# Kernel tuning notes

Measured on AMD Instinct MI355X. Metric: run time of the kernel, lower is better.

The kernel has to match this reference:

```python
import jax, jax.numpy as jnp
import numpy as np

B, S, D, A = 32, 2048, 512, 256


def setup_inputs() -> dict:
    key = jax.random.key(0)
    ks = jax.random.split(key, 9)
    enc = jax.random.normal(ks[0], (B, S, D), dtype=jnp.float32)
    dec = jax.random.normal(ks[1], (B, 1, D), dtype=jnp.float32)
    prev = jax.random.uniform(ks[2], (B, S), dtype=jnp.float32)
    prev = prev / jnp.sum(prev, axis=1, keepdims=True)  # normalized prev attention
    noise = jax.random.normal(ks[3], (B, S), dtype=jnp.float32)
    W = jax.random.normal(ks[4], (A, D), dtype=jnp.float32) / np.sqrt(D)
    V = jax.random.normal(ks[5], (A, D), dtype=jnp.float32) / np.sqrt(D)
    b = jax.random.normal(ks[6], (A,), dtype=jnp.float32)
    v_w = jax.random.normal(ks[7], (1, A), dtype=jnp.float32)
    v_g = jnp.full((1,), np.sqrt(1.0 / A), dtype=jnp.float32)  # weight_norm g init
    v_bias = jax.random.normal(ks[8], (1,), dtype=jnp.float32)
    r = jnp.full((1,), -4.0, dtype=jnp.float32)
    return {"encoder_outputs": enc, "decoder_h": dec, "prev_alpha": prev,
            "noise": noise, "W": W, "V": V, "b": b, "v_w": v_w,
            "v_g": v_g, "v_bias": v_bias, "r": r}


def reference(encoder_outputs, decoder_h, prev_alpha, noise, W, V, b, v_w, v_g, v_bias, r):
    # Energy: tanh-MLP Bahdanau score with weight-normed output projection
    h = jnp.tanh(jnp.einsum('bsd,ad->bsa', encoder_outputs, W)
                 + jnp.einsum('bod,ad->boa', decoder_h, V)  # [B,1,A] broadcasts over S
                 + b)
    w_eff = v_g * v_w / jnp.linalg.norm(v_w)       # weight_norm: g * v / ||v||
    energy = jnp.einsum('bsa,oa->bso', h, w_eff)[..., 0] + v_bias[0] + r[0]  # [B,S]
    # Soft monotonic attention recurrence
    p_select = jax.nn.sigmoid(energy + noise)
    log1mp = jnp.log(jnp.clip(1.0 - p_select, 1e-10, 1.0))
    cumprod_1mp = jnp.exp(jnp.cumsum(log1mp, axis=1))  # safe_cumprod
    alpha = p_select * cumprod_1mp * jnp.cumsum(prev_alpha / cumprod_1mp, axis=1)
    # Context: enc^T @ alpha
    context = jnp.einsum('bsd,bs->bd', encoder_outputs, alpha)
    return context, alpha
```

## Files before the change

kernel.cpp:

```cpp
#include <hip/hip_runtime.h>
#include <math.h>

#define B_  32
#define S_  2048
#define D_  512
#define A_  256
#define BS_ (B_ * S_)

#define WEFF_OFF  0
#define DEC_OFF   256
#define EPART_OFF 8448
#define CTX_OFF   (8448 + BS_)

typedef _Float16 f16x8 __attribute__((ext_vector_type(8)));
typedef __fp16   fp16x2 __attribute__((ext_vector_type(2)));
typedef _Float16 half4 __attribute__((ext_vector_type(4)));
typedef float floatx4 __attribute__((ext_vector_type(4)));

__device__ __forceinline__ void glds16(const void* g, void* l) {
    __builtin_amdgcn_global_load_lds(
        (const __attribute__((address_space(1))) void*)g,
        (__attribute__((address_space(3))) void*)l, 16, 0, 0);
}

__global__ void ma_prep_kernel(const float* __restrict__ v_w,
                               const float* __restrict__ v_g,
                               const float* __restrict__ dec,
                               const float* __restrict__ V,
                               const float* __restrict__ bvec,
                               const float* __restrict__ W,
                               _Float16* __restrict__ W16,
                               float* __restrict__ ws) {
    __shared__ float sh[D_];
    const int bid = blockIdx.x, t = threadIdx.x;
    if (bid == 0) {
        float v = v_w[t];
        float sq = v * v;
        #pragma unroll
        for (int off = 32; off > 0; off >>= 1) sq += __shfl_down(sq, off, 64);
        if ((t & 63) == 0) sh[t >> 6] = sq;
        __syncthreads();
        float n2 = sh[0] + sh[1] + sh[2] + sh[3];
        ws[WEFF_OFF + t] = v_g[0] * v / sqrtf(n2);
    } else if (bid <= B_) {
        const int b = bid - 1;
        sh[t]       = dec[b * D_ + t];
        sh[t + 256] = dec[b * D_ + 256 + t];
        __syncthreads();
        const float4* Vr = (const float4*)(V + (size_t)t * D_);
        float acc = 0.f;
        #pragma unroll 4
        for (int k = 0; k < D_ / 4; ++k) {
            float4 v4 = Vr[k];
            acc = fmaf(v4.x, sh[4*k+0], acc);
            acc = fmaf(v4.y, sh[4*k+1], acc);
            acc = fmaf(v4.z, sh[4*k+2], acc);
            acc = fmaf(v4.w, sh[4*k+3], acc);
        }
        ws[DEC_OFF + b * A_ + t] = acc + bvec[t];
    } else {
        int i = (bid - (B_ + 1)) * 256 + t;
        float4 v = ((const float4*)W)[i];
        half4 h;
        h[0] = (_Float16)v.x; h[1] = (_Float16)v.y;
        h[2] = (_Float16)v.z; h[3] = (_Float16)v.w;
        ((half4*)W16)[i] = h;
    }
}

__global__ __launch_bounds__(512) void ma_energy_mfma(
        const float* __restrict__ enc,
        const _Float16* __restrict__ W16,
        const float* __restrict__ ws_in,
        float* __restrict__ energy) {
    __shared__ __align__(16) char smem[81920];
    float*    const Asm = (float*)smem;
    _Float16* const Bsm = (_Float16*)(smem + 49152);

    const int t  = threadIdx.x;
    const int bx = blockIdx.x;
    const size_t R0 = (size_t)bx * 128;
    const int batch = bx >> 4;

    const int lane = t & 63, wid = t >> 6;
    const int wm = wid >> 2, wn = wid & 3;
    const int fr = lane & 15, kq = lane >> 4;

    const int arow = t >> 3, ac = t & 7;
    const float* AgS0 = enc + (R0 + (size_t)arow) * D_ + (ac ^ (arow & 7)) * 4;
    const float* AgS1 = AgS0 + (size_t)64 * D_;
    const int brow = t >> 2, bc = t & 3;
    const _Float16* BgS0 = W16 + (size_t)brow * D_ + (bc ^ ((brow >> 1) & 3)) * 8;
    const _Float16* BgS1 = BgS0 + (size_t)128 * D_;

    const int axc0 = ((2 * kq)     ^ (fr & 7)) * 4;
    const int axc1 = ((2 * kq + 1) ^ (fr & 7)) * 4;
    const int bxo  = (kq ^ ((fr >> 1) & 3)) * 8;

    floatx4 acc[4][4];
    #pragma unroll
    for (int m = 0; m < 4; ++m)
        #pragma unroll
        for (int n = 0; n < 4; ++n) acc[m][n] = (floatx4)0.f;

#define STAGE_A(kt, buf) do { \
        glds16(AgS0 + (kt) * 32, Asm + (buf) * 4096 + wid * 256); \
        glds16(AgS1 + (kt) * 32, Asm + (buf) * 4096 + wid * 256 + 2048); } while (0)
#define STAGE_B(kt, buf) do { \
        glds16(BgS0 + (kt) * 32, Bsm + (buf) * 8192 + wid * 512); \
        glds16(BgS1 + (kt) * 32, Bsm + (buf) * 8192 + wid * 512 + 4096); } while (0)

#define COMPUTE(ca, cb) do { \
        const float*    Abuf = Asm + (ca) * 4096; \
        const _Float16* Bbuf = Bsm + (cb) * 8192; \
        f16x8 af[4], bf[4]; \
        _Pragma("unroll") \
        for (int m = 0; m < 4; ++m) { \
            const int rbase = (wm * 64 + m * 16 + fr) * 32; \
            float4 lo = *(const float4*)&Abuf[rbase + axc0]; \
            float4 hi = *(const float4*)&Abuf[rbase + axc1]; \
            union { fp16x2 h2[4]; f16x8 v; } u; \
            u.h2[0] = __builtin_amdgcn_cvt_pkrtz(lo.x, lo.y); \
            u.h2[1] = __builtin_amdgcn_cvt_pkrtz(lo.z, lo.w); \
            u.h2[2] = __builtin_amdgcn_cvt_pkrtz(hi.x, hi.y); \
            u.h2[3] = __builtin_amdgcn_cvt_pkrtz(hi.z, hi.w); \
            af[m] = u.v; \
        } \
        _Pragma("unroll") \
        for (int n = 0; n < 4; ++n) \
            bf[n] = *(const f16x8*)&Bbuf[(wn * 64 + n * 16 + fr) * 32 + bxo]; \
        _Pragma("unroll") \
        for (int m = 0; m < 4; ++m) \
            _Pragma("unroll") \
            for (int n = 0; n < 4; ++n) \
                acc[m][n] = __builtin_amdgcn_mfma_f32_16x16x32_f16(af[m], bf[n], acc[m][n], 0, 0, 0); \
    } while (0)

    STAGE_A(0, 0); STAGE_B(0, 0);
    STAGE_A(1, 1); STAGE_B(1, 1);
    STAGE_A(2, 2);
    asm volatile("s_waitcnt vmcnt(6)" ::: "memory");
    __builtin_amdgcn_s_barrier();
    __builtin_amdgcn_sched_barrier(0);

    int ca = 0, cb = 0;
    #pragma unroll 1
    for (int kt = 0; kt < 13; ++kt) {
        COMPUTE(ca, cb);
        __builtin_amdgcn_s_barrier();
        STAGE_B(kt + 2, cb);
        STAGE_A(kt + 3, ca);
        asm volatile("s_waitcnt vmcnt(6)" ::: "memory");
        __builtin_amdgcn_s_barrier();
        __builtin_amdgcn_sched_barrier(0);
        ca = (ca == 2) ? 0 : ca + 1;
        cb ^= 1;
    }
    COMPUTE(1, 1);
    __builtin_amdgcn_s_barrier();
    STAGE_B(15, 1);
    asm volatile("s_waitcnt vmcnt(4)" ::: "memory");
    __builtin_amdgcn_s_barrier();
    __builtin_amdgcn_sched_barrier(0);
    COMPUTE(2, 0);
    __builtin_amdgcn_s_barrier();
    asm volatile("s_waitcnt vmcnt(0)" ::: "memory");
    __builtin_amdgcn_s_barrier();
    __builtin_amdgcn_sched_barrier(0);
    COMPUTE(0, 1);
    __syncthreads();

    float* const red = (float*)smem;
    const float* weff  = ws_in + WEFF_OFF;
    const float* dterm = ws_in + DEC_OFF + batch * A_;
    float wj[4], dj[4];
    #pragma unroll
    for (int n = 0; n < 4; ++n) {
        int a = wn * 64 + n * 16 + fr;
        wj[n] = weff[a];
        dj[n] = dterm[a];
    }
    #pragma unroll
    for (int m = 0; m < 4; ++m) {
        #pragma unroll
        for (int r = 0; r < 4; ++r) {
            float v = 0.f;
            #pragma unroll
            for (int n = 0; n < 4; ++n) {
                float x = acc[m][n][r] + dj[n];
                float e = __expf(2.f * x);
                v += (1.f - 2.f / (e + 1.f)) * wj[n];
            }
            #pragma unroll
            for (int mask = 1; mask < 16; mask <<= 1)
                v += __shfl_xor(v, mask, 64);
            if (fr == 0)
                red[wn * 128 + wm * 64 + m * 16 + (kq << 2) + r] = v;
        }
    }
    __syncthreads();
    if (t < 128)
        energy[R0 + t] = red[t] + red[128 + t] + red[256 + t] + red[384 + t];
#undef STAGE_A
#undef STAGE_B
#undef COMPUTE
}

__global__ void ma_scan_kernel(const float* __restrict__ energy,
                               const float* __restrict__ noise,
                               const float* __restrict__ prev,
                               const float* __restrict__ v_bias,
                               const float* __restrict__ r,
                               float* __restrict__ alpha_out) {
    int b = blockIdx.x, t = threadIdx.x;
    const float bias = v_bias[0] + r[0];
    int base = b * S_ + t * 8;
    float p[8], av[8], bv[8];
    #pragma unroll
    for (int i = 0; i < 8; ++i) {
        float e = energy[base + i] + bias + noise[base + i];
        float pi = 1.f / (1.f + expf(-e));
        p[i]  = pi;
        av[i] = fmaxf(1.f - pi, 1e-10f);
        bv[i] = prev[base + i];
    }
    float Ai = 1.f, Bi = 0.f;
    #pragma unroll
    for (int i = 0; i < 8; ++i) { Bi = av[i] * Bi + bv[i]; Ai *= av[i]; }
    int lane = t & 63;
    #pragma unroll
    for (int off = 1; off < 64; off <<= 1) {
        float Ap = __shfl_up(Ai, off, 64);
        float Bp = __shfl_up(Bi, off, 64);
        if (lane >= off) { Bi = Ai * Bp + Bi; Ai = Ai * Ap; }
    }
    __shared__ float wA[4], wB[4];
    int w = t >> 6;
    if (lane == 63) { wA[w] = Ai; wB[w] = Bi; }
    __syncthreads();
    float Ax = __shfl_up(Ai, 1, 64);
    float Bx = __shfl_up(Bi, 1, 64);
    if (lane == 0) { Ax = 1.f; Bx = 0.f; }
    float PwA = 1.f, PwB = 0.f;
    for (int q = 0; q < w; ++q) { PwB = wA[q] * PwB + wB[q]; PwA *= wA[q]; }
    float T = Ax * PwB + Bx;
    #pragma unroll
    for (int i = 0; i < 8; ++i) {
        T = av[i] * T + bv[i];
        alpha_out[base + i] = p[i] * T;
    }
}

__global__ void ma_ctxpart_kernel(const float* __restrict__ enc,
                                  const float* __restrict__ alpha,
                                  float* __restrict__ cpart) {
    int b = blockIdx.x, sc = blockIdx.y, t = threadIdx.x;
    const int sp = t >> 7;
    const int d4 = t & 127;
    const float4* e = (const float4*)(enc + ((size_t)b * S_ + sc * 64) * D_);
    const float* al = alpha + b * S_ + sc * 64;
    float4 acc = {0.f, 0.f, 0.f, 0.f};
    #pragma unroll 4
    for (int s = sp; s < 64; s += 2) {
        float a = al[s];
        float4 v = e[(size_t)s * 128 + d4];
        acc.x = fmaf(v.x, a, acc.x);
        acc.y = fmaf(v.y, a, acc.y);
        acc.z = fmaf(v.z, a, acc.z);
        acc.w = fmaf(v.w, a, acc.w);
    }
    __shared__ float4 sh[128];
    if (sp == 1) sh[d4] = acc;
    __syncthreads();
    if (sp == 0) {
        float4 o = sh[d4];
        acc.x += o.x; acc.y += o.y; acc.z += o.z; acc.w += o.w;
        ((float4*)(cpart + ((size_t)(sc * B_ + b)) * D_))[d4] = acc;
    }
}

__global__ void ma_ctxreduce_kernel(const float* __restrict__ cpart,
                                    float* __restrict__ ctx) {
    int b = blockIdx.x, t = threadIdx.x;
    #pragma unroll
    for (int h = 0; h < 2; ++h) {
        int d = t + h * 256;
        float s = 0.f;
        #pragma unroll
        for (int q = 0; q < 32; ++q) s += cpart[((size_t)(q * B_ + b)) * D_ + d];
        ctx[b * D_ + d] = s;
    }
}

extern "C" void kernel_launch(void* const* d_in, const int* in_sizes, int n_in,
                              void* d_out, int out_size, void* d_ws, size_t ws_size,
                              hipStream_t stream) {
    const float* enc    = (const float*)d_in[0];
    const float* dec    = (const float*)d_in[1];
    const float* prev   = (const float*)d_in[2];
    const float* noise  = (const float*)d_in[3];
    const float* W      = (const float*)d_in[4];
    const float* V      = (const float*)d_in[5];
    const float* bvec   = (const float*)d_in[6];
    const float* v_w    = (const float*)d_in[7];
    const float* v_g    = (const float*)d_in[8];
    const float* v_bias = (const float*)d_in[9];
    const float* r      = (const float*)d_in[10];

    float* out = (float*)d_out;
    float* ws  = (float*)d_ws;
    float* alpha = out + B_ * D_;
    _Float16* W16 = (_Float16*)(ws + CTX_OFF);

    ma_prep_kernel<<<1 + B_ + 128, 256, 0, stream>>>(v_w, v_g, dec, V, bvec, W, W16, ws);
    ma_energy_mfma<<<512, 512, 0, stream>>>(enc, W16, ws, ws + EPART_OFF);
    ma_scan_kernel<<<B_, 256, 0, stream>>>(ws + EPART_OFF, noise, prev, v_bias, r, alpha);
    dim3 gc(B_, 32);
    ma_ctxpart_kernel<<<gc, 256, 0, stream>>>(enc, alpha, ws + CTX_OFF);
    ma_ctxreduce_kernel<<<B_, 256, 0, stream>>>(ws + CTX_OFF, out);
}
```

Baseline: 78.28 us.

## Load encoder tiles directly to registers and stage W16 in two large phases

The energy GEMM no longer stages encoder rows through LDS. Each wave loads its fp32 A fragments straight from global memory into double-buffered registers, prefetching two k-steps ahead. W16 is loaded into a 128KB swizzled LDS buffer in two halves instead of a triple/double ring with fine-grained waitcnt barriers, and launch bounds request 2 blocks per CU. This cuts LDS traffic and barrier count, but it raises register pressure and the large LDS footprint may limit occupancy.

```diff
diff --git a/kernel.cpp b/kernel.cpp
--- a/kernel.cpp
+++ b/kernel.cpp
@@ -68,14 +68,12 @@
     }
 }
 
-__global__ __launch_bounds__(512) void ma_energy_mfma(
+__global__ __launch_bounds__(512, 2) void ma_energy_mfma(
         const float* __restrict__ enc,
         const _Float16* __restrict__ W16,
         const float* __restrict__ ws_in,
         float* __restrict__ energy) {
-    __shared__ __align__(16) char smem[81920];
-    float*    const Asm = (float*)smem;
-    _Float16* const Bsm = (_Float16*)(smem + 49152);
+    __shared__ __align__(16) _Float16 Bsm[65536];
 
     const int t  = threadIdx.x;
     const int bx = blockIdx.x;
@@ -86,16 +84,7 @@
     const int wm = wid >> 2, wn = wid & 3;
     const int fr = lane & 15, kq = lane >> 4;
 
-    const int arow = t >> 3, ac = t & 7;
-    const float* AgS0 = enc + (R0 + (size_t)arow) * D_ + (ac ^ (arow & 7)) * 4;
-    const float* AgS1 = AgS0 + (size_t)64 * D_;
-    const int brow = t >> 2, bc = t & 3;
-    const _Float16* BgS0 = W16 + (size_t)brow * D_ + (bc ^ ((brow >> 1) & 3)) * 8;
-    const _Float16* BgS1 = BgS0 + (size_t)128 * D_;
-
-    const int axc0 = ((2 * kq)     ^ (fr & 7)) * 4;
-    const int axc1 = ((2 * kq + 1) ^ (fr & 7)) * 4;
-    const int bxo  = (kq ^ ((fr >> 1) & 3)) * 8;
+    const float* Ag = enc + (R0 + wm * 64 + (size_t)fr) * D_ + kq * 8;
 
     floatx4 acc[4][4];
     #pragma unroll
@@ -103,32 +92,40 @@
         #pragma unroll
         for (int n = 0; n < 4; ++n) acc[m][n] = (floatx4)0.f;
 
-#define STAGE_A(kt, buf) do { \
-        glds16(AgS0 + (kt) * 32, Asm + (buf) * 4096 + wid * 256); \
-        glds16(AgS1 + (kt) * 32, Asm + (buf) * 4096 + wid * 256 + 2048); } while (0)
-#define STAGE_B(kt, buf) do { \
-        glds16(BgS0 + (kt) * 32, Bsm + (buf) * 8192 + wid * 512); \
-        glds16(BgS1 + (kt) * 32, Bsm + (buf) * 8192 + wid * 512 + 4096); } while (0)
-
-#define COMPUTE(ca, cb) do { \
-        const float*    Abuf = Asm + (ca) * 4096; \
-        const _Float16* Bbuf = Bsm + (cb) * 8192; \
+#define STAGEB(phase) do { \
+        _Pragma("unroll") \
+        for (int j = 0; j < 16; ++j) { \
+            const int p   = (wid * 16 + j) * 64 + lane; \
+            const int row = p >> 5, cc = p & 31; \
+            glds16(W16 + (size_t)row * D_ + (phase) * 256 + ((cc ^ (row & 7)) * 8), \
+                   &Bsm[(wid * 16 + j) * 512]); \
+        } } while (0)
+
+#define LOADA(buf, gk) do { \
+        _Pragma("unroll") \
+        for (int m = 0; m < 4; ++m) { \
+            buf[m][0] = *(const float4*)(Ag + m * 16 * D_ + (gk) * 32); \
+            buf[m][1] = *(const float4*)(Ag + m * 16 * D_ + (gk) * 32 + 4); \
+        } } while (0)
+
+#define SUBITER(buf, kt, gk) do { \
         f16x8 af[4], bf[4]; \
         _Pragma("unroll") \
         for (int m = 0; m < 4; ++m) { \
-            const int rbase = (wm * 64 + m * 16 + fr) * 32; \
-            float4 lo = *(const float4*)&Abuf[rbase + axc0]; \
-            float4 hi = *(const float4*)&Abuf[rbase + axc1]; \
             union { fp16x2 h2[4]; f16x8 v; } u; \
-            u.h2[0] = __builtin_amdgcn_cvt_pkrtz(lo.x, lo.y); \
-            u.h2[1] = __builtin_amdgcn_cvt_pkrtz(lo.z, lo.w); \
-            u.h2[2] = __builtin_amdgcn_cvt_pkrtz(hi.x, hi.y); \
-            u.h2[3] = __builtin_amdgcn_cvt_pkrtz(hi.z, hi.w); \
+            u.h2[0] = __builtin_amdgcn_cvt_pkrtz(buf[m][0].x, buf[m][0].y); \
+            u.h2[1] = __builtin_amdgcn_cvt_pkrtz(buf[m][0].z, buf[m][0].w); \
+            u.h2[2] = __builtin_amdgcn_cvt_pkrtz(buf[m][1].x, buf[m][1].y); \
+            u.h2[3] = __builtin_amdgcn_cvt_pkrtz(buf[m][1].z, buf[m][1].w); \
             af[m] = u.v; \
         } \
-        _Pragma("unroll") \
-        for (int n = 0; n < 4; ++n) \
-            bf[n] = *(const f16x8*)&Bbuf[(wn * 64 + n * 16 + fr) * 32 + bxo]; \
+        if ((gk) + 2 < 16) LOADA(buf, (gk) + 2); \
+        _Pragma("unroll") \
+        for (int n = 0; n < 4; ++n) { \
+            const int row = wn * 64 + n * 16 + fr; \
+            const int cc  = (kt) * 4 + kq; \
+            bf[n] = *(const f16x8*)&Bsm[row * 256 + ((cc ^ (row & 7)) * 8)]; \
+        } \
         _Pragma("unroll") \
         for (int m = 0; m < 4; ++m) \
             _Pragma("unroll") \
@@ -136,41 +133,27 @@
                 acc[m][n] = __builtin_amdgcn_mfma_f32_16x16x32_f16(af[m], bf[n], acc[m][n], 0, 0, 0); \
     } while (0)
 
-    STAGE_A(0, 0); STAGE_B(0, 0);
-    STAGE_A(1, 1); STAGE_B(1, 1);
-    STAGE_A(2, 2);
-    asm volatile("s_waitcnt vmcnt(6)" ::: "memory");
-    __builtin_amdgcn_s_barrier();
-    __builtin_amdgcn_sched_barrier(0);
-
-    int ca = 0, cb = 0;
-    #pragma unroll 1
-    for (int kt = 0; kt < 13; ++kt) {
-        COMPUTE(ca, cb);
-        __builtin_amdgcn_s_barrier();
-        STAGE_B(kt + 2, cb);
-        STAGE_A(kt + 3, ca);
-        asm volatile("s_waitcnt vmcnt(6)" ::: "memory");
-        __builtin_amdgcn_s_barrier();
-        __builtin_amdgcn_sched_barrier(0);
-        ca = (ca == 2) ? 0 : ca + 1;
-        cb ^= 1;
-    }
-    COMPUTE(1, 1);
-    __builtin_amdgcn_s_barrier();
-    STAGE_B(15, 1);
-    asm volatile("s_waitcnt vmcnt(4)" ::: "memory");
-    __builtin_amdgcn_s_barrier();
-    __builtin_amdgcn_sched_barrier(0);
-    COMPUTE(2, 0);
-    __builtin_amdgcn_s_barrier();
-    asm volatile("s_waitcnt vmcnt(0)" ::: "memory");
-    __builtin_amdgcn_s_barrier();
-    __builtin_amdgcn_sched_barrier(0);
-    COMPUTE(0, 1);
+    float4 pA[4][2], pB[4][2];
+    LOADA(pA, 0);
+    LOADA(pB, 1);
+
+    #pragma unroll
+    for (int phase = 0; phase < 2; ++phase) {
+        if (phase) __syncthreads();
+        STAGEB(phase);
+        __syncthreads();
+        #pragma unroll
+        for (int kh = 0; kh < 4; ++kh) {
+            SUBITER(pA, 2 * kh,     phase * 8 + 2 * kh);
+            SUBITER(pB, 2 * kh + 1, phase * 8 + 2 * kh + 1);
+        }
+    }
+#undef STAGEB
+#undef LOADA
+#undef SUBITER
+
     __syncthreads();
-
-    float* const red = (float*)smem;
+    float* const red = (float*)Bsm;
     const float* weff  = ws_in + WEFF_OFF;
     const float* dterm = ws_in + DEC_OFF + batch * A_;
     float wj[4], dj[4];
@@ -201,9 +184,6 @@
     __syncthreads();
     if (t < 128)
         energy[R0 + t] = red[t] + red[128 + t] + red[256 + t] + red[384 + t];
-#undef STAGE_A
-#undef STAGE_B
-#undef COMPUTE
 }
 
 __global__ void ma_scan_kernel(const float* __restrict__ energy,
```

Measured after the change: 123.5 us. 1.58x slower.
